# Optimization experiments

Measured on AMD Instinct MI355X. Metric: run time of the kernel, lower is better.

Reference implementation:

```python
import jax, jax.numpy as jnp
import numpy as np

B, T = 1, 1024
HID = 2048
H, HKV, D = 16, 4, 128
G = H // HKV          # kv groups
TOPK = 256
HI, DI = 4, 32        # indexer heads / head dim


def _rotate_half(x):
    x1, x2 = jnp.split(x, 2, axis=-1)
    return jnp.concatenate([-x2, x1], axis=-1)


def _apply_rotary(x, cos, sin):
    # x: (B,T,H,D), cos/sin: (1,T,1,D)
    return x * cos + _rotate_half(x) * sin


def _rms_norm(x):
    eps = jnp.finfo(x.dtype).eps
    return x * jax.lax.rsqrt(jnp.mean(x * x, axis=-1, keepdims=True) + eps)


def setup_inputs() -> dict:
    key = jax.random.key(0)
    ks = jax.random.split(key, 9)
    s = 0.02
    x = jax.random.normal(ks[0], (B, T, HID), jnp.float32)
    # rotary tables
    inv_freq = 1.0 / (10000.0 ** (jnp.arange(0, D, 2, dtype=jnp.float32) / D))
    freqs = jnp.outer(jnp.arange(T, dtype=jnp.float32), inv_freq)   # (T, D/2)
    emb = jnp.concatenate([freqs, freqs], axis=-1)                  # (T, D)
    cos = jnp.cos(emb)[None, :, None, :]
    sin = jnp.sin(emb)[None, :, None, :]
    Wq = jax.random.normal(ks[1], (HID, H * D), jnp.float32) * s
    Wk = jax.random.normal(ks[2], (HID, HKV * D), jnp.float32) * s
    Wv = jax.random.normal(ks[3], (HID, HKV * D), jnp.float32) * s
    Wo = jax.random.normal(ks[4], (H * D, HID), jnp.float32) * s
    Wqi = jax.random.normal(ks[5], (HID, HI * DI), jnp.float32) * s
    Wwi = jax.random.normal(ks[6], (HID, HI), jnp.float32) * s
    Wki = jax.random.normal(ks[7], (HID, DI), jnp.float32) * s
    return {"x": x, "cos": cos, "sin": sin, "Wq": Wq, "Wk": Wk, "Wv": Wv,
            "Wo": Wo, "Wqi": Wqi, "Wwi": Wwi, "Wki": Wki}


def reference(x, cos, sin, Wq, Wk, Wv, Wo, Wqi, Wwi, Wki):
    b, t, _ = x.shape
    q = (x @ Wq).reshape(b, t, H, D)
    k = (x @ Wk).reshape(b, t, HKV, D)
    v = (x @ Wv).reshape(b, t, HKV, D)
    q = _rms_norm(_apply_rotary(q, cos, sin))
    k = _rms_norm(_apply_rotary(k, cos, sin))

    # ---- lightning indexer: I[t,s] = sum_j w[t,j] * relu(q_i[t,j] . k_i[s]) ----
    qi = (x @ Wqi).reshape(b, t, HI, DI)
    wi = x @ Wwi                                   # (B,T,HI)
    ki = x @ Wki                                   # (B,T,DI)
    raw = jax.nn.relu(jnp.einsum('bthd,bsd->bths', qi, ki))
    idx_scores = jnp.einsum('bths,bth->bts', raw, wi)     # (B,T,T)

    pos = jnp.arange(t)
    causal = pos[None, :] <= pos[:, None]                 # (T,T) valid s<=t
    masked = jnp.where(causal[None], idx_scores, -jnp.inf)
    _, top_idx = jax.lax.top_k(masked, TOPK)              # (B,T,K) int32

    # gather selected K/V: (B,T,K,HKV,D)
    gather = jax.vmap(lambda arr, idx: arr[idx])          # per-batch fancy gather
    sel_k = gather(k, top_idx)
    sel_v = gather(v, top_idx)
    sel_mask = top_idx <= pos[None, :, None]              # (B,T,K)

    # grouped-query attention over selected tokens (avoid repeat_interleave)
    q5 = q.reshape(b, t, HKV, G, D)                       # q head h -> kv head h//G
    scale = D ** -0.5
    scores = jnp.einsum('btngd,btknd->btngk', q5, sel_k) * scale
    scores = jnp.where(sel_mask[:, :, None, None, :], scores, -jnp.inf)
    probs = jax.nn.softmax(scores, axis=-1)
    attn = jnp.einsum('btngk,btknd->btngd', probs, sel_v)  # (B,T,HKV,G,D)
    out = attn.reshape(b, t, H * D) @ Wo
    return out
```

## Files before the change

### kernel.cpp

```cpp
#include <hip/hip_runtime.h>
#include <hip/hip_bf16.h>
#include <math.h>

#define T_    1024
#define HID_  2048
#define NH    16
#define NKV   4
#define DH    128
#define TOPK_ 256
#define HI_   4
#define DI_   32
#define NPROJ 3072
#define NIDX  164
#define KSPLIT 8
#define KCHUNK 256

#ifndef INFINITY
#define INFINITY (__builtin_inff())
#endif

typedef __attribute__((ext_vector_type(8))) short bf16x8;
typedef __attribute__((ext_vector_type(4))) float f32x4;

__device__ inline unsigned int packbf(float f) {
    unsigned int u = __float_as_uint(f);
    return (u + 0x7fffu + ((u >> 16) & 1u)) >> 16;
}

#define GLDS16(g, l) __builtin_amdgcn_global_load_lds( \
    (const __attribute__((address_space(1))) void*)(g), \
    (__attribute__((address_space(3))) void*)(l), 16, 0, 0)

__device__ inline void tcast_body(const float* __restrict__ W, unsigned short* __restrict__ Wt,
                                  int N, int bx, int by, int tid, float (*tile)[33]) {
    const int n0 = bx * 32, k0 = by * 32;
    const int tx = tid & 31, ty = tid >> 5;
#pragma unroll
    for (int i = 0; i < 4; ++i)
        tile[ty + i * 8][tx] = W[(size_t)(k0 + ty + i * 8) * N + (n0 + tx)];
    __syncthreads();
#pragma unroll
    for (int i = 0; i < 4; ++i) {
        int n = n0 + ty + i * 8;
        Wt[(size_t)n * HID_ + k0 + tx] = (unsigned short)packbf(tile[tx][ty + i * 8]);
    }
}

__device__ inline void gemm64_body(const unsigned short* __restrict__ A,
                                   const unsigned short* __restrict__ Bt,
                                   float* __restrict__ C, int K, int ldc,
                                   int bx, int by, int tid,
                                   unsigned short* As, unsigned short* Bs) {
    const int lane = tid & 63, w = tid >> 6;
    const int wr = w >> 1, wc = w & 1;
    const int brow = by * 64, bcol = bx * 64;
    const int l15 = lane & 15, lq = lane >> 4;

    f32x4 acc[2][2] = {};

    const int srow = tid >> 3;
    const int gsrc = ((tid & 7) ^ (srow & 7)) * 8;
    const unsigned short* ga  = A  + (size_t)(brow + srow) * K + gsrc;
    const unsigned short* ga2 = ga + (size_t)32 * K;
    const unsigned short* gb  = Bt + (size_t)(bcol + srow) * K + gsrc;
    const unsigned short* gb2 = gb + (size_t)32 * K;
    unsigned short* la  = &As[(size_t)tid * 8];
    unsigned short* la2 = &As[(size_t)(tid + 256) * 8];
    unsigned short* lb  = &Bs[(size_t)tid * 8];
    unsigned short* lb2 = &Bs[(size_t)(tid + 256) * 8];

    for (int k0 = 0; k0 < K; k0 += 64) {
        GLDS16(ga + k0,  la);
        GLDS16(ga2 + k0, la2);
        GLDS16(gb + k0,  lb);
        GLDS16(gb2 + k0, lb2);
        __syncthreads();
        bf16x8 fa[2][2], fb[2][2];
#pragma unroll
        for (int m = 0; m < 2; ++m)
#pragma unroll
            for (int kk = 0; kk < 2; ++kk) {
                int row = wr * 32 + m * 16 + l15;
                fa[m][kk] = *(const bf16x8*)&As[row * 64 + (((kk * 4 + lq) ^ (l15 & 7)) * 8)];
            }
#pragma unroll
        for (int nn = 0; nn < 2; ++nn)
#pragma unroll
            for (int kk = 0; kk < 2; ++kk) {
                int row = wc * 32 + nn * 16 + l15;
                fb[nn][kk] = *(const bf16x8*)&Bs[row * 64 + (((kk * 4 + lq) ^ (l15 & 7)) * 8)];
            }
#pragma unroll
        for (int kk = 0; kk < 2; ++kk)
#pragma unroll
            for (int m = 0; m < 2; ++m)
#pragma unroll
                for (int nn = 0; nn < 2; ++nn)
                    acc[m][nn] = __builtin_amdgcn_mfma_f32_16x16x32_bf16(fa[m][kk], fb[nn][kk], acc[m][nn], 0, 0, 0);
        __syncthreads();
    }
#pragma unroll
    for (int m = 0; m < 2; ++m)
#pragma unroll
        for (int nn = 0; nn < 2; ++nn)
#pragma unroll
            for (int q = 0; q < 4; ++q) {
                int row = brow + wr * 32 + m * 16 + lq * 4 + q;
                int col = bcol + wc * 32 + nn * 16 + l15;
                C[(size_t)row * ldc + col] = acc[m][nn][q];
            }
}

__global__ __launch_bounds__(256) void prep1(const float* __restrict__ x,
                                             const float* __restrict__ Wq,
                                             const float* __restrict__ Wk,
                                             const float* __restrict__ Wv,
                                             const float* __restrict__ Wqi,
                                             const float* __restrict__ Wwi,
                                             const float* __restrict__ Wki,
                                             unsigned short* __restrict__ xb,
                                             unsigned short* __restrict__ WtAll,
                                             float* __restrict__ Wi) {
    __shared__ float tile[32][33];
    int bid = blockIdx.x;
    const int tid = threadIdx.x;
    if (bid < 4096) { tcast_body(Wq, WtAll, HID_, bid & 63, bid >> 6, tid, tile); return; }
    bid -= 4096;
    if (bid < 1024) { tcast_body(Wk, WtAll + (size_t)2048 * HID_, 512, bid & 15, bid >> 4, tid, tile); return; }
    bid -= 1024;
    if (bid < 1024) { tcast_body(Wv, WtAll + (size_t)2560 * HID_, 512, bid & 15, bid >> 4, tid, tile); return; }
    bid -= 1024;
    if (bid < 1024) {
        int e = bid * 256 + tid;
        const float4* p = (const float4*)(x + (size_t)e * 8);
        float4 a = p[0], b = p[1];
        uint4 r;
        r.x = packbf(a.x) | (packbf(a.y) << 16);
        r.y = packbf(a.z) | (packbf(a.w) << 16);
        r.z = packbf(b.x) | (packbf(b.y) << 16);
        r.w = packbf(b.z) | (packbf(b.w) << 16);
        *(uint4*)(xb + (size_t)e * 8) = r;
        return;
    }
    bid -= 1024;
    {
        int e = bid * 256 + tid;
        if (e >= HID_ * NIDX) return;
        int k = e / NIDX, c = e - k * NIDX;
        float v;
        if (c < 128) v = Wqi[(size_t)k * 128 + c];
        else if (c < 132) v = Wwi[(size_t)k * 4 + (c - 128)];
        else v = Wki[(size_t)k * 32 + (c - 132)];
        Wi[e] = v;
    }
}

__global__ __launch_bounds__(256) void fusedA(const unsigned short* __restrict__ xb,
                                              const unsigned short* __restrict__ WtAll,
                                              float* __restrict__ proj,
                                              const float* __restrict__ x,
                                              const float* __restrict__ Wi,
                                              float* __restrict__ Cpart) {
    __shared__ __align__(16) char smem[64 * 64 * 2 * 2];
    const int tid = threadIdx.x;
    int bid = blockIdx.x;

    if (bid < 768) {
        unsigned short* As = (unsigned short*)smem;
        unsigned short* Bs = As + 64 * 64;
        gemm64_body(xb, WtAll, proj, HID_, NPROJ, bid % 48, bid / 48, tid, As, Bs);
        return;
    }
    float (*As2)[68] = (float(*)[68])smem;
    float (*Bs2)[68] = As2 + 16;
    int s = bid - 768;
    const int bx = s % 3, by = (s / 3) % 16, z = s / 48;
    const int tx = tid & 15, ty = tid >> 4;
    const int brow = by * 64, bcol = bx * 64;
    const int kbeg = z * KCHUNK, kend = kbeg + KCHUNK;
    const int M = T_, N = NIDX, K = HID_;

    const int ar = tid >> 2, ac4 = (tid & 3) * 4;
    const int br = tid >> 4, bc4 = (tid & 15) * 4;

    float acc[4][4];
#pragma unroll
    for (int i = 0; i < 4; ++i)
#pragma unroll
        for (int j = 0; j < 4; ++j) acc[i][j] = 0.f;

    for (int k0 = kbeg; k0 < kend; k0 += 16) {
        float4 va = *(const float4*)&x[(size_t)(brow + ar) * K + k0 + ac4];
        float4 vb;
        int col = bcol + bc4;
        if (col <= N - 4) vb = *(const float4*)&Wi[(size_t)(k0 + br) * N + col];
        else vb = (float4){0.f, 0.f, 0.f, 0.f};
        As2[ac4 + 0][ar] = va.x;
        As2[ac4 + 1][ar] = va.y;
        As2[ac4 + 2][ar] = va.z;
        As2[ac4 + 3][ar] = va.w;
        *(float4*)&Bs2[br][bc4] = vb;
        __syncthreads();
#pragma unroll
        for (int kk = 0; kk < 16; ++kk) {
            float4 a4 = *(const float4*)&As2[kk][ty * 4];
            float4 b4 = *(const float4*)&Bs2[kk][tx * 4];
            float a[4] = {a4.x, a4.y, a4.z, a4.w};
            float b[4] = {b4.x, b4.y, b4.z, b4.w};
#pragma unroll
            for (int i = 0; i < 4; ++i)
#pragma unroll
                for (int j = 0; j < 4; ++j) acc[i][j] += a[i] * b[j];
        }
        __syncthreads();
    }
#pragma unroll
    for (int i = 0; i < 4; ++i) {
        int r = brow + ty * 4 + i;
#pragma unroll
        for (int j = 0; j < 4; ++j) {
            int c = bcol + tx * 4 + j;
            if (c < N) Cpart[((size_t)z * M + r) * N + c] = acc[i][j];
        }
    }
}

__global__ __launch_bounds__(256) void reduce_k(const float* __restrict__ Cpart,
                                                float* __restrict__ Cout,
                                                float* __restrict__ kib, int MN) {
    int e = blockIdx.x * 256 + threadIdx.x;
    if (e >= MN) return;
    float s = 0.f;
#pragma unroll
    for (int z = 0; z < KSPLIT; ++z) s += Cpart[(size_t)z * MN + e];
    Cout[e] = s;
    int t = e / NIDX, c = e - t * NIDX;
    if (c >= 132) kib[(size_t)t * DI_ + (c - 132)] = s;
}

__global__ __launch_bounds__(256) void fusedB(const float* __restrict__ proj,
                                              const float* __restrict__ cosb,
                                              const float* __restrict__ sinb,
                                              unsigned short* __restrict__ qbb,
                                              unsigned short* __restrict__ kbb,
                                              unsigned int* __restrict__ vbb,
                                              const float* __restrict__ Wo,
                                              unsigned short* __restrict__ Wot,
                                              const float* __restrict__ proji,
                                              const float* __restrict__ kib,
                                              int* __restrict__ idxout) {
    __shared__ float tile[32][33];
    const int tid = threadIdx.x;
    int bid = blockIdx.x;

    if (bid < 5376) {
        const int w = tid >> 6, lane = tid & 63;
        const int u = bid * 4 + w;
        const int t = u / 21, h = u - t * 21;
        if (h < 20) {
            const float* row;
            unsigned short* dst;
            if (h < 16) { row = proj + (size_t)t * NPROJ + h * DH;               dst = qbb + ((size_t)t * NH + h) * DH; }
            else        { row = proj + (size_t)t * NPROJ + HID_ + (h - 16) * DH; dst = kbb + ((size_t)t * NKV + (h - 16)) * DH; }
            float a = row[lane], b = row[lane + 64];
            float c0 = cosb[t * DH + lane],      s0 = sinb[t * DH + lane];
            float c1 = cosb[t * DH + lane + 64], s1 = sinb[t * DH + lane + 64];
            float r0 = a * c0 - b * s0;
            float r1 = b * c1 + a * s1;
            float ss = r0 * r0 + r1 * r1;
#pragma unroll
            for (int o = 32; o > 0; o >>= 1) ss += __shfl_xor(ss, o);
            float inv = rsqrtf(ss * (1.0f / 128.0f) + 1.1920929e-07f);
            dst[lane]      = (unsigned short)packbf(r0 * inv);
            dst[lane + 64] = (unsigned short)packbf(r1 * inv);
        } else {
            const float* src = proj + (size_t)t * NPROJ + HID_ + 512;
#pragma unroll
            for (int i = 0; i < 4; ++i) {
                int c2 = lane + i * 64;
                vbb[(size_t)t * 256 + c2] = packbf(src[2 * c2]) | (packbf(src[2 * c2 + 1]) << 16);
            }
        }
        return;
    }
    bid -= 5376;
    if (bid < 4096) {
        tcast_body(Wo, Wot, HID_, bid & 63, bid >> 6, tid, tile);
        return;
    }
    bid -= 4096;
    {
        const int t = bid;
        int* orow = idxout + (size_t)t * TOPK_;
        if (t < TOPK_) { orow[tid] = tid; return; }

        __shared__ float qsh[128];
        __shared__ float wsh[4];
        if (tid < 128) qsh[tid] = proji[(size_t)t * NIDX + tid];
        else if (tid < 132) wsh[tid - 128] = proji[(size_t)t * NIDX + tid];
        __syncthreads();

        const int n = t + 1;
        const int lane = tid & 63, wave = tid >> 6;

        unsigned int key[4];
#pragma unroll
        for (int j = 0; j < 4; ++j) {
            int s = j * 256 + tid;
            if (s < n) {
                const float4* kr = (const float4*)&kib[(size_t)s * DI_];
                float4 k4[8];
#pragma unroll
                for (int d4 = 0; d4 < 8; ++d4) k4[d4] = kr[d4];
                float sc = 0.f;
#pragma unroll
                for (int h = 0; h < HI_; ++h) {
                    float d = 0.f;
#pragma unroll
                    for (int d4 = 0; d4 < 8; ++d4) {
                        const float* qp = &qsh[h * 32 + d4 * 4];
                        d += k4[d4].x * qp[0] + k4[d4].y * qp[1] +
                             k4[d4].z * qp[2] + k4[d4].w * qp[3];
                    }
                    sc += wsh[h] * fmaxf(d, 0.f);
                }
                unsigned int u = __float_as_uint(sc);
                key[j] = (u & 0x80000000u) ? ~u : (u | 0x80000000u);
            } else key[j] = 0u;
        }

        __shared__ int wcnt[2][4];
        unsigned int prefix = 0;
#pragma unroll 1
        for (int b = 31; b >= 0; --b) {
            unsigned int cand = prefix | (1u << b);
            int c = (key[0] >= cand) + (key[1] >= cand) + (key[2] >= cand) + (key[3] >= cand);
#pragma unroll
            for (int o = 32; o > 0; o >>= 1) c += __shfl_xor(c, o);
            if (lane == 0) wcnt[b & 1][wave] = c;
            __syncthreads();
            int total = wcnt[b & 1][0] + wcnt[b & 1][1] + wcnt[b & 1][2] + wcnt[b & 1][3];
            if (total >= TOPK_) prefix = cand;
        }
        const unsigned int T = prefix;

        __shared__ int posc;
        __shared__ int eqtot[4][4];
        __syncthreads();
        {
            int c = (key[0] > T) + (key[1] > T) + (key[2] > T) + (key[3] > T);
#pragma unroll
            for (int o = 32; o > 0; o >>= 1) c += __shfl_xor(c, o);
            if (lane == 0) wcnt[0][wave] = c;
        }
        if (tid == 0) posc = 0;

        int e[4]; int myp[4];
#pragma unroll
        for (int j = 0; j < 4; ++j) {
            e[j] = (key[j] == T) ? 1 : 0;
            unsigned long long m = __ballot(e[j]);
            myp[j] = __popcll(m & ((1ull << lane) - 1ull));
            if (lane == 0) eqtot[j][wave] = __popcll(m);
        }
        __syncthreads();
        const int cntGT = wcnt[0][0] + wcnt[0][1] + wcnt[0][2] + wcnt[0][3];
        const int need = TOPK_ - cntGT;

#pragma unroll
        for (int j = 0; j < 4; ++j)
            if (key[j] > T) {
                int p = atomicAdd(&posc, 1);
                orow[p] = j * 256 + tid;
            }
        int runbase = 0;
#pragma unroll
        for (int j = 0; j < 4; ++j) {
            int wavebase = 0;
#pragma unroll
            for (int w2 = 0; w2 < 4; ++w2) if (w2 < wave) wavebase += eqtot[j][w2];
            int g = runbase + wavebase + myp[j];
            if (e[j] && g < need) orow[cntGT + g] = j * 256 + tid;
            runbase += eqtot[j][0] + eqtot[j][1] + eqtot[j][2] + eqtot[j][3];
        }
    }
}

__global__ __launch_bounds__(256) void gemm64(const unsigned short* __restrict__ A,
                                              const unsigned short* __restrict__ Bt,
                                              float* __restrict__ C,
                                              int K, int ldc) {
    __shared__ unsigned short As[64 * 64];
    __shared__ unsigned short Bs[64 * 64];
    gemm64_body(A, Bt, C, K, ldc, blockIdx.x, blockIdx.y, threadIdx.x, As, Bs);
}

__global__ __launch_bounds__(256) void attn3(const unsigned short* __restrict__ qbb,
                                             const unsigned short* __restrict__ kbb,
                                             const unsigned short* __restrict__ vbb,
                                             const int* __restrict__ idx,
                                             unsigned short* __restrict__ attnb) {
    const int t = blockIdx.x, n = blockIdx.y;
    const int tid = threadIdx.x, lane = tid & 63, w = tid >> 6;
    const int C = (t + 1 < TOPK_) ? t + 1 : TOPK_;
    const int l15 = lane & 15, lq = lane >> 4;

    __shared__ int sidx[TOPK_];
    __shared__ float sinv[4];
    __shared__ unsigned short P[16][264];
    __shared__ __align__(16) char spvs[64 * 136 * 2];
    float (*sp)[TOPK_] = (float(*)[TOPK_])spvs;
    unsigned short (*Vs)[136] = (unsigned short(*)[136])spvs;

    sidx[tid] = idx[(size_t)t * TOPK_ + tid];
    __syncthreads();

    const size_t qrow = (size_t)t * NH + n * 4 + (l15 < 4 ? l15 : 3);
    bf16x8 qf[4];
#pragma unroll
    for (int ks = 0; ks < 4; ++ks)
        qf[ks] = *(const bf16x8*)&qbb[qrow * DH + ks * 32 + lq * 8];

#pragma unroll
    for (int tt = 0; tt < 4; ++tt) {
        const int tile = w * 4 + tt;
        const int tok = tile * 16 + l15;
        const unsigned short* krow = &kbb[((size_t)sidx[tok] * NKV + n) * DH];
        f32x4 acc = {0.f, 0.f, 0.f, 0.f};
        __builtin_amdgcn_s_setprio(1);
#pragma unroll
        for (int ks = 0; ks < 4; ++ks) {
            bf16x8 yf = *(const bf16x8*)&krow[ks * 32 + lq * 8];
            acc = __builtin_amdgcn_mfma_f32_16x16x32_bf16(qf[ks], yf, acc, 0, 0, 0);
        }
        __builtin_amdgcn_s_setprio(0);
        if (lane < 16) {
            int j = tile * 16 + lane;
            bool ok = j < C;
#pragma unroll
            for (int q = 0; q < 4; ++q)
                sp[q][j] = ok ? acc[q] * 0.08838834764831845f : -INFINITY;
        }
    }
    __syncthreads();

    {
        float v0 = sp[w][lane], v1 = sp[w][lane + 64],
              v2 = sp[w][lane + 128], v3 = sp[w][lane + 192];
        float m = fmaxf(fmaxf(v0, v1), fmaxf(v2, v3));
#pragma unroll
        for (int o = 32; o > 0; o >>= 1) m = fmaxf(m, __shfl_xor(m, o));
        float e0 = expf(v0 - m), e1 = expf(v1 - m), e2 = expf(v2 - m), e3 = expf(v3 - m);
        float sum = e0 + e1 + e2 + e3;
#pragma unroll
        for (int o = 32; o > 0; o >>= 1) sum += __shfl_xor(sum, o);
        if (lane == 0) sinv[w] = 1.f / sum;
        P[w][lane]       = (unsigned short)packbf(e0);
        P[w][lane + 64]  = (unsigned short)packbf(e1);
        P[w][lane + 128] = (unsigned short)packbf(e2);
        P[w][lane + 192] = (unsigned short)packbf(e3);
    }

    f32x4 pacc[2] = {};
#pragma unroll 1
    for (int tau = 0; tau < 4; ++tau) {
        __syncthreads();
#pragma unroll
        for (int it = 0; it < 4; ++it) {
            int c = tid + it * 256;
            int r = c >> 4, doff = (c & 15) * 8;
            int col = doff ^ (((r >> 3) & 3) << 4);
            *(uint4*)&Vs[r][col] =
                *(const uint4*)&vbb[((size_t)sidx[tau * 64 + r] * NKV + n) * DH + doff];
        }
        __syncthreads();
#pragma unroll
        for (int kk = 0; kk < 2; ++kk) {
            bf16x8 xf = *(const bf16x8*)&P[l15][tau * 64 + kk * 32 + lq * 8];
            const int colr0 = ((2 * w + 0) * 16 + l15) ^ (lq << 4);
            const int colr1 = ((2 * w + 1) * 16 + l15) ^ (lq << 4);
            bf16x8 yf0, yf1;
#pragma unroll
            for (int j = 0; j < 8; ++j) {
                yf0[j] = (short)Vs[kk * 32 + lq * 8 + j][colr0];
                yf1[j] = (short)Vs[kk * 32 + lq * 8 + j][colr1];
            }
            __builtin_amdgcn_s_setprio(1);
            pacc[0] = __builtin_amdgcn_mfma_f32_16x16x32_bf16(xf, yf0, pacc[0], 0, 0, 0);
            pacc[1] = __builtin_amdgcn_mfma_f32_16x16x32_bf16(xf, yf1, pacc[1], 0, 0, 0);
            __builtin_amdgcn_s_setprio(0);
        }
    }

    if (lane < 16) {
#pragma unroll
        for (int dt = 0; dt < 2; ++dt)
#pragma unroll
            for (int q = 0; q < 4; ++q)
                attnb[(size_t)(t * NH + n * 4 + q) * DH + (2 * w + dt) * 16 + l15] =
                    (unsigned short)packbf(pacc[dt][q] * sinv[q]);
    }
}

extern "C" void kernel_launch(void* const* d_in, const int* in_sizes, int n_in,
                              void* d_out, int out_size, void* d_ws, size_t ws_size,
                              hipStream_t stream) {
    const float* x    = (const float*)d_in[0];
    const float* cosb = (const float*)d_in[1];
    const float* sinb = (const float*)d_in[2];
    const float* Wq   = (const float*)d_in[3];
    const float* Wk   = (const float*)d_in[4];
    const float* Wv   = (const float*)d_in[5];
    const float* Wo   = (const float*)d_in[6];
    const float* Wqi  = (const float*)d_in[7];
    const float* Wwi  = (const float*)d_in[8];
    const float* Wki  = (const float*)d_in[9];
    float* out = (float*)d_out;

    unsigned short* xb    = (unsigned short*)d_ws;
    unsigned short* WtAll = xb + 2097152;
    float*  proj  = (float*)(WtAll + 6291456);
    float*  Wi    = proj + 3145728;
    float*  proji = Wi + 335872;
    float*  kib   = proji + 167936;
    int*    idxb  = (int*)(kib + 1048576);
    unsigned short* kbb   = (unsigned short*)(idxb + 262144);
    unsigned short* vbb   = kbb + 524288;
    unsigned short* attnb = vbb + 524288;
    unsigned short* Wot   = WtAll;
    unsigned short* qbb   = xb;
    float* Cpart = (float*)kbb;

    prep1<<<dim3(8480), dim3(256), 0, stream>>>(x, Wq, Wk, Wv, Wqi, Wwi, Wki, xb, WtAll, Wi);

    fusedA<<<dim3(1152), dim3(256), 0, stream>>>(xb, WtAll, proj, x, Wi, Cpart);

    reduce_k<<<dim3((T_ * NIDX + 255) / 256), dim3(256), 0, stream>>>(Cpart, proji, kib, T_ * NIDX);

    fusedB<<<dim3(10496), dim3(256), 0, stream>>>(proj, cosb, sinb, qbb, kbb, (unsigned int*)vbb,
                                                  Wo, Wot, proji, kib, idxb);

    attn3<<<dim3(T_, NKV), dim3(256), 0, stream>>>(qbb, kbb, vbb, idxb, attnb);

    gemm64<<<dim3(HID_ / 64, T_ / 64), dim3(256), 0, stream>>>(attnb, Wot, out, HID_, HID_);
}
```

Measured before the change: 172.6 us.

## Double-buffer V staging in attention with async global-to-LDS loads

Reworks the attention kernel's V loading into a two-buffer LDS pipeline. The first V tile is prefetched during the QK/softmax phase, and later tiles are staged with direct global-to-LDS copies (GLDS16) while the current tile feeds the MFMAs. The goal is to hide gather latency and drop one barrier per iteration. In exchange the kernel uses more shared memory (separate sp and two 16KB V buffers), which may lower occupancy. It also shrinks P to 4 rows, relies on a GLDS16 macro defined elsewhere, and puts the swizzle on the global source address.

```diff
diff --git a/kernel.cpp b/kernel.cpp
--- a/kernel.cpp
+++ b/kernel.cpp
@@ -395,7 +395,7 @@
     gemm64_body(A, Bt, C, K, ldc, blockIdx.x, blockIdx.y, threadIdx.x, As, Bs);
 }
 
-__global__ __launch_bounds__(256) void attn3(const unsigned short* __restrict__ qbb,
+__global__ __launch_bounds__(256) void attn6(const unsigned short* __restrict__ qbb,
                                              const unsigned short* __restrict__ kbb,
                                              const unsigned short* __restrict__ vbb,
                                              const int* __restrict__ idx,
@@ -406,14 +406,27 @@
     const int l15 = lane & 15, lq = lane >> 4;
 
     __shared__ int sidx[TOPK_];
+    __shared__ float sp[4][TOPK_];
     __shared__ float sinv[4];
-    __shared__ unsigned short P[16][264];
-    __shared__ __align__(16) char spvs[64 * 136 * 2];
-    float (*sp)[TOPK_] = (float(*)[TOPK_])spvs;
-    unsigned short (*Vs)[136] = (unsigned short(*)[136])spvs;
+    __shared__ unsigned short P[4][264];
+    __shared__ unsigned short Vs[2][64 * 128];
 
     sidx[tid] = idx[(size_t)t * TOPK_ + tid];
     __syncthreads();
+
+    const int sr0 = tid >> 4, sdoff = (tid & 15) * 8;
+#define STAGE_V(buf, tau)                                                          \
+    {                                                                              \
+        _Pragma("unroll")                                                          \
+        for (int it = 0; it < 4; ++it) {                                           \
+            int r = sr0 + it * 16;                                                 \
+            int gs = sdoff ^ (((r >> 3) & 3) << 4);                                \
+            GLDS16(&vbb[((size_t)sidx[(tau) * 64 + r] * NKV + n) * DH + gs],       \
+                   &Vs[buf][(size_t)(tid + it * 256) * 8]);                        \
+        }                                                                          \
+    }
+
+    STAGE_V(0, 0);
 
     const size_t qrow = (size_t)t * NH + n * 4 + (l15 < 4 ? l15 : 3);
     bf16x8 qf[4];
@@ -460,37 +473,34 @@
         P[w][lane + 128] = (unsigned short)packbf(e2);
         P[w][lane + 192] = (unsigned short)packbf(e3);
     }
-
+    __syncthreads();
+
+    const int prow = (l15 < 4) ? l15 : 3;
     f32x4 pacc[2] = {};
-#pragma unroll 1
+#pragma unroll
     for (int tau = 0; tau < 4; ++tau) {
-        __syncthreads();
-#pragma unroll
-        for (int it = 0; it < 4; ++it) {
-            int c = tid + it * 256;
-            int r = c >> 4, doff = (c & 15) * 8;
-            int col = doff ^ (((r >> 3) & 3) << 4);
-            *(uint4*)&Vs[r][col] =
-                *(const uint4*)&vbb[((size_t)sidx[tau * 64 + r] * NKV + n) * DH + doff];
-        }
-        __syncthreads();
+        const unsigned short* Vb = Vs[tau & 1];
+        if (tau < 3) STAGE_V((tau + 1) & 1, tau + 1);
 #pragma unroll
         for (int kk = 0; kk < 2; ++kk) {
-            bf16x8 xf = *(const bf16x8*)&P[l15][tau * 64 + kk * 32 + lq * 8];
+            bf16x8 xf = *(const bf16x8*)&P[prow][tau * 64 + kk * 32 + lq * 8];
             const int colr0 = ((2 * w + 0) * 16 + l15) ^ (lq << 4);
             const int colr1 = ((2 * w + 1) * 16 + l15) ^ (lq << 4);
+            const int tokb = kk * 32 + lq * 8;
             bf16x8 yf0, yf1;
 #pragma unroll
             for (int j = 0; j < 8; ++j) {
-                yf0[j] = (short)Vs[kk * 32 + lq * 8 + j][colr0];
-                yf1[j] = (short)Vs[kk * 32 + lq * 8 + j][colr1];
+                yf0[j] = (short)Vb[(tokb + j) * 128 + colr0];
+                yf1[j] = (short)Vb[(tokb + j) * 128 + colr1];
             }
             __builtin_amdgcn_s_setprio(1);
             pacc[0] = __builtin_amdgcn_mfma_f32_16x16x32_bf16(xf, yf0, pacc[0], 0, 0, 0);
             pacc[1] = __builtin_amdgcn_mfma_f32_16x16x32_bf16(xf, yf1, pacc[1], 0, 0, 0);
             __builtin_amdgcn_s_setprio(0);
         }
-    }
+        __syncthreads();
+    }
+#undef STAGE_V
 
     if (lane < 16) {
 #pragma unroll
@@ -540,7 +550,7 @@
     fusedB<<<dim3(10496), dim3(256), 0, stream>>>(proj, cosb, sinb, qbb, kbb, (unsigned int*)vbb,
                                                   Wo, Wot, proji, kib, idxb);
 
-    attn3<<<dim3(T_, NKV), dim3(256), 0, stream>>>(qbb, kbb, vbb, idxb, attnb);
+    attn6<<<dim3(T_, NKV), dim3(256), 0, stream>>>(qbb, kbb, vbb, idxb, attnb);
 
     gemm64<<<dim3(HID_ / 64, T_ / 64), dim3(256), 0, stream>>>(attnb, Wot, out, HID_, HID_);
 }
```

Measured after the change: 170.4 us. No clear change (-1.3%).
